# Kernel tuning notes

Hardware: AMD Instinct MI355X
Metric: run time of the kernel (lower is better)

Reference implementation:

```python
import jax, jax.numpy as jnp
import numpy as np

B, Q, S, H = 2048, 128, 128, 32  # batch, num slices, slice length, hidden dim
C = Q * S


def setup_inputs() -> dict:
    key = jax.random.key(0)
    k0, k1, k2 = jax.random.split(key, 3)
    x = jax.random.normal(k0, (B, 1, 1, C), dtype=jnp.float32)
    # stacked per-slice MLP params (Glorot-ish scaling)
    W1 = jax.random.normal(k1, (Q, S, H), dtype=jnp.float32) * (1.0 / np.sqrt(S))
    b1 = jnp.zeros((Q, H), dtype=jnp.float32)
    W2 = jax.random.normal(k2, (Q, H, 1), dtype=jnp.float32) * (1.0 / np.sqrt(H))
    b2 = jnp.zeros((Q, 1), dtype=jnp.float32)
    return {"x": x, "W1": W1, "b1": b1, "W2": W2, "b2": b2}


def reference(x, W1, b1, W2, b2):
    # (B,1,1,C) -> (B,Q,S): slice the channel dim into Q groups
    xs = x.reshape(x.shape[0], Q, -1)
    # per-slice Dense(H) with ELU: grouped GEMM over the Q axis
    h = jax.nn.elu(jnp.einsum("bqs,qsh->bqh", xs, W1) + b1)  # (B,Q,H)
    # per-slice Dense(1): contract hidden dim -> scalar per slice
    out = jnp.einsum("bqh,qh->bq", h, W2[..., 0]) + b2[..., 0]  # (B,Q)
    return out
```

## Files before the change

### kernel.cpp

```cpp
#include <hip/hip_runtime.h>
#include <hip/hip_bf16.h>
#include <math.h>

#define QN 128
#define SN 128
#define HN 32
#define CN (QN * SN)
#define TILE_R 128

using half8   = __attribute__((ext_vector_type(8))) _Float16;
using floatx4 = __attribute__((ext_vector_type(4))) float;

__global__ __launch_bounds__(256, 4)
void divenc_kernel(const float* __restrict__ x,
                   const float* __restrict__ W1,
                   const float* __restrict__ b1,
                   const float* __restrict__ W2,
                   const float* __restrict__ b2,
                   float* __restrict__ out) {
  const int q    = blockIdx.y;
  const int b0   = blockIdx.x * TILE_R;
  const int tid  = threadIdx.x;
  const int lane = tid & 63;
  const int wid  = __builtin_amdgcn_readfirstlane(tid >> 6);
  const int nA   = lane & 15;
  const int koct = lane >> 4;

  const float* __restrict__ w1q = W1 + (size_t)q * (SN * HN);
  half8 bf[2][4];
  #pragma unroll
  for (int n0 = 0; n0 < 2; ++n0) {
    #pragma unroll
    for (int kk = 0; kk < 4; ++kk) {
      #pragma unroll
      for (int i = 0; i < 8; ++i) {
        const int k = kk * 32 + koct * 8 + i;
        bf[n0][kk][i] = (_Float16)w1q[k * HN + n0 * 16 + nA];
      }
    }
  }

  floatx4 z = {0.f, 0.f, 0.f, 0.f};
  floatx4 acc[2][2];
  acc[0][0] = z; acc[0][1] = z; acc[1][0] = z; acc[1][1] = z;

  const int row0 = b0 + wid * 32;
  #pragma unroll
  for (int mt = 0; mt < 2; ++mt) {
    const float* __restrict__ rp =
        x + (size_t)(row0 + mt * 16 + nA) * CN + q * SN + koct * 8;
    #pragma unroll
    for (int kk = 0; kk < 4; ++kk) {
      const float4 va = *reinterpret_cast<const float4*>(rp + kk * 32);
      const float4 vb = *reinterpret_cast<const float4*>(rp + kk * 32 + 4);
      half8 af;
      af[0] = (_Float16)va.x; af[1] = (_Float16)va.y;
      af[2] = (_Float16)va.z; af[3] = (_Float16)va.w;
      af[4] = (_Float16)vb.x; af[5] = (_Float16)vb.y;
      af[6] = (_Float16)vb.z; af[7] = (_Float16)vb.w;
      acc[mt][0] = __builtin_amdgcn_mfma_f32_16x16x32_f16(af, bf[0][kk], acc[mt][0], 0, 0, 0);
      acc[mt][1] = __builtin_amdgcn_mfma_f32_16x16x32_f16(af, bf[1][kk], acc[mt][1], 0, 0, 0);
    }
  }

  const float b1a = b1[q * HN + nA],  b1b = b1[q * HN + 16 + nA];
  const float w2a = W2[q * HN + nA],  w2b = W2[q * HN + 16 + nA];
  const float b2q = b2[q];

  #pragma unroll
  for (int mt = 0; mt < 2; ++mt) {
    #pragma unroll
    for (int reg = 0; reg < 4; ++reg) {
      float v0 = acc[mt][0][reg] + b1a;
      v0 = v0 > 0.f ? v0 : expm1f(v0);
      float v1 = acc[mt][1][reg] + b1b;
      v1 = v1 > 0.f ? v1 : expm1f(v1);
      float t = fmaf(v0, w2a, v1 * w2b);
      t += __shfl_xor(t, 1);
      t += __shfl_xor(t, 2);
      t += __shfl_xor(t, 4);
      t += __shfl_xor(t, 8);
      if (nA == 0) {
        const int row = row0 + mt * 16 + koct * 4 + reg;
        out[(size_t)row * QN + q] = t + b2q;
      }
    }
  }
}

extern "C" void kernel_launch(void* const* d_in, const int* in_sizes, int n_in,
                              void* d_out, int out_size, void* d_ws, size_t ws_size,
                              hipStream_t stream) {
  const float* x  = (const float*)d_in[0];
  const float* W1 = (const float*)d_in[1];
  const float* b1 = (const float*)d_in[2];
  const float* W2 = (const float*)d_in[3];
  const float* b2 = (const float*)d_in[4];
  float* out = (float*)d_out;

  const int B = in_sizes[0] / CN;
  dim3 grid(B / TILE_R, QN);
  divenc_kernel<<<grid, 256, 0, stream>>>(x, W1, b1, W2, b2, out);
}
```

Measured before the change: 31.77 us.

## Stage x tiles through LDS with coalesced loads, each wave handles one slice

The block tile is changed from 128 rows of one slice to 32 rows by 4 slices. x is loaded with fully coalesced float4 reads (2KB contiguous per row), converted to fp16 and written to padded LDS. Each wave then reads its slice's A fragments from LDS. The aim is to replace the scattered 32-byte global reads with contiguous ones, at the cost of about 35KB of LDS per block, a barrier, and W1 now being loaded by 4 times as many blocks.

Result: no change. 31.94 us (+0.5%).

```diff
diff --git a/kernel.cpp b/kernel.cpp
--- a/kernel.cpp
+++ b/kernel.cpp
@@ -6,9 +6,12 @@
 #define SN 128
 #define HN 32
 #define CN (QN * SN)
-#define TILE_R 128
+#define RB 32
+#define QB 4
+#define LROW 136
 
 using half8   = __attribute__((ext_vector_type(8))) _Float16;
+using half4v  = __attribute__((ext_vector_type(4))) _Float16;
 using floatx4 = __attribute__((ext_vector_type(4))) float;
 
 __global__ __launch_bounds__(256, 4)
@@ -18,13 +21,34 @@
                    const float* __restrict__ W2,
                    const float* __restrict__ b2,
                    float* __restrict__ out) {
-  const int q    = blockIdx.y;
-  const int b0   = blockIdx.x * TILE_R;
+  const int q0   = blockIdx.y * QB;
+  const int r0   = blockIdx.x * RB;
   const int tid  = threadIdx.x;
   const int lane = tid & 63;
   const int wid  = __builtin_amdgcn_readfirstlane(tid >> 6);
+  const int q    = q0 + wid;
   const int nA   = lane & 15;
   const int koct = lane >> 4;
+
+  __shared__ _Float16 xs[QB * RB * LROW];
+
+  {
+    const float* xb = x + (size_t)r0 * CN + (size_t)q0 * SN;
+    #pragma unroll
+    for (int i = 0; i < 16; ++i) {
+      const int f  = i * 256 + tid;
+      const int r  = f >> 7;
+      const int su = f & 127;
+      const int qi = su >> 5;
+      const int c  = su & 31;
+      const float4 v = *reinterpret_cast<const float4*>(
+          xb + (size_t)r * CN + qi * SN + c * 4);
+      half4v h;
+      h[0] = (_Float16)v.x; h[1] = (_Float16)v.y;
+      h[2] = (_Float16)v.z; h[3] = (_Float16)v.w;
+      *reinterpret_cast<half4v*>(&xs[qi * (RB * LROW) + r * LROW + c * 4]) = h;
+    }
+  }
 
   const float* __restrict__ w1q = W1 + (size_t)q * (SN * HN);
   half8 bf[2][4];
@@ -39,33 +63,28 @@
       }
     }
   }
+  const float b1a = b1[q * HN + nA],  b1b = b1[q * HN + 16 + nA];
+  const float w2a = W2[q * HN + nA],  w2b = W2[q * HN + 16 + nA];
+  const float b2q = b2[q];
 
-  floatx4 z = {0.f, 0.f, 0.f, 0.f};
+  __syncthreads();
+
+  const _Float16* myq = &xs[wid * (RB * LROW)];
+  const floatx4 z = {0.f, 0.f, 0.f, 0.f};
   floatx4 acc[2][2];
   acc[0][0] = z; acc[0][1] = z; acc[1][0] = z; acc[1][1] = z;
 
-  const int row0 = b0 + wid * 32;
   #pragma unroll
   for (int mt = 0; mt < 2; ++mt) {
-    const float* __restrict__ rp =
-        x + (size_t)(row0 + mt * 16 + nA) * CN + q * SN + koct * 8;
+    const _Float16* rowb = myq + (mt * 16 + nA) * LROW;
     #pragma unroll
     for (int kk = 0; kk < 4; ++kk) {
-      const float4 va = *reinterpret_cast<const float4*>(rp + kk * 32);
-      const float4 vb = *reinterpret_cast<const float4*>(rp + kk * 32 + 4);
-      half8 af;
-      af[0] = (_Float16)va.x; af[1] = (_Float16)va.y;
-      af[2] = (_Float16)va.z; af[3] = (_Float16)va.w;
-      af[4] = (_Float16)vb.x; af[5] = (_Float16)vb.y;
-      af[6] = (_Float16)vb.z; af[7] = (_Float16)vb.w;
+      const half8 af = *reinterpret_cast<const half8*>(
+          rowb + (kk * 4 + koct) * 8);
       acc[mt][0] = __builtin_amdgcn_mfma_f32_16x16x32_f16(af, bf[0][kk], acc[mt][0], 0, 0, 0);
       acc[mt][1] = __builtin_amdgcn_mfma_f32_16x16x32_f16(af, bf[1][kk], acc[mt][1], 0, 0, 0);
     }
   }
-
-  const float b1a = b1[q * HN + nA],  b1b = b1[q * HN + 16 + nA];
-  const float w2a = W2[q * HN + nA],  w2b = W2[q * HN + 16 + nA];
-  const float b2q = b2[q];
 
   #pragma unroll
   for (int mt = 0; mt < 2; ++mt) {
@@ -81,7 +100,7 @@
       t += __shfl_xor(t, 4);
       t += __shfl_xor(t, 8);
       if (nA == 0) {
-        const int row = row0 + mt * 16 + koct * 4 + reg;
+        const int row = r0 + mt * 16 + koct * 4 + reg;
         out[(size_t)row * QN + q] = t + b2q;
       }
     }
@@ -99,6 +118,6 @@
   float* out = (float*)d_out;
 
   const int B = in_sizes[0] / CN;
-  dim3 grid(B / TILE_R, QN);
+  dim3 grid(B / RB, QN / QB);
   divenc_kernel<<<grid, 256, 0, stream>>>(x, W1, b1, W2, b2, out);
 }
```
